# Kernel tuning notes

Measured on AMD Instinct MI355X. Metric: run time of the kernel, lower is better.

## Reference

```python
import jax, jax.numpy as jnp
import numpy as np

B_FACTOR = 4          # branching factor of the complete tree
DEPTH = 7             # levels 0..DEPTH; level DEPTH are leaves
N_NODES = (B_FACTOR ** (DEPTH + 1) - 1) // (B_FACTOR - 1)   # 21845
N_INTERNAL = (B_FACTOR ** DEPTH - 1) // (B_FACTOR - 1)      # 5461
IN_SIZE = 512
HID = 512
PARAM_SCALE = 0.02


def setup_inputs() -> dict:
    key = jax.random.key(0)
    ks = jax.random.split(key, 7)
    x = jax.random.normal(ks[0], (N_NODES, IN_SIZE), dtype=jnp.float32)
    # torch nn.Linear parameters: y = x @ W.T + b
    W_iou = jax.random.normal(ks[1], (3 * HID, IN_SIZE), dtype=jnp.float32) * PARAM_SCALE
    b_iou = jax.random.normal(ks[2], (3 * HID,), dtype=jnp.float32) * PARAM_SCALE
    W_f = jax.random.normal(ks[3], (HID, IN_SIZE), dtype=jnp.float32) * PARAM_SCALE
    b_f = jax.random.normal(ks[4], (HID,), dtype=jnp.float32) * PARAM_SCALE
    U_iou = jax.random.normal(ks[5], (3 * HID, HID), dtype=jnp.float32) * PARAM_SCALE
    U_f = jax.random.normal(ks[6], (HID, HID), dtype=jnp.float32) * PARAM_SCALE
    # children[j] = indices of the 4 children of internal node j (complete 4-ary tree)
    children = (B_FACTOR * jnp.arange(N_INTERNAL, dtype=jnp.int32)[:, None]
                + jnp.arange(1, B_FACTOR + 1, dtype=jnp.int32)[None, :])
    return {"x": x, "children": children, "W_iou": W_iou, "b_iou": b_iou,
            "W_f": W_f, "b_f": b_f, "U_iou": U_iou, "U_f": U_f}


def reference(x, children, W_iou, b_iou, W_f, b_f, U_iou, U_f):
    """Child-Sum Tree-LSTM over a complete 4-ary tree, processed level-batched
    bottom-up (equivalent to the per-node postorder recursion in the source).
    Leaves keep h = c = 0, as in the source (_forward_postorder returns early).
    NOTE: the source applies NO sigmoid to the forget gate term; we keep that.
    """
    N = x.shape[0]
    H = U_f.shape[0]
    # input-dependent parts are tree-independent: precompute once for all nodes
    wx_iou = x @ W_iou.T + b_iou          # [N, 3H]
    wx_f = x @ W_f.T + b_f                # [N, H]
    h = jnp.zeros((N, H), dtype=x.dtype)
    c = jnp.zeros_like(h)
    # level l occupies node indices [offs[l], offs[l+1]) — static constants
    offs = [(B_FACTOR ** l - 1) // (B_FACTOR - 1) for l in range(DEPTH + 2)]
    for l in range(DEPTH - 1, -1, -1):    # internal levels, deepest first
        s, e = offs[l], offs[l + 1]
        ch = children[s:e]                # [M, 4]
        h_ch = h[ch]                      # [M, 4, H] gather of child hidden states
        c_ch = c[ch]                      # [M, 4, H]
        h_sum = h_ch.sum(axis=1)          # child-sum
        iou = wx_iou[s:e] + h_sum @ U_iou.T               # [M, 3H]
        i, o, u = jnp.split(iou, 3, axis=-1)
        i = jax.nn.sigmoid(i)
        o = jax.nn.sigmoid(o)
        u = jnp.tanh(u)
        # forget term per child (no sigmoid, faithful to source)
        f = wx_f[s:e][:, None, :] + h_ch @ U_f.T          # [M, 4, H]
        c_new = i * u + (f * c_ch).sum(axis=1)            # [M, H]
        h = h.at[s:e].set(o * jnp.tanh(c_new))
        c = c.at[s:e].set(c_new)
    return h, c
```

## Files before the change

kernel.cpp:

```cpp
#include <hip/hip_runtime.h>
#include <cmath>

constexpr int N_NODES = 21845;
constexpr int N_INT   = 5461;
constexpr int HID     = 512;

typedef short  short8  __attribute__((ext_vector_type(8)));
typedef float  floatx4 __attribute__((ext_vector_type(4)));

__device__ __forceinline__ unsigned short f2bf(float f) {
    unsigned int u = __float_as_uint(f);
    u += 0x7fffu + ((u >> 16) & 1u);
    return (unsigned short)(u >> 16);
}

__global__ void prep_kernel(const float* __restrict__ x,
                            const float* __restrict__ W_iou,
                            const float* __restrict__ W_f,
                            const float* __restrict__ U_iou,
                            const float* __restrict__ U_f,
                            float* __restrict__ h_leaf,
                            float* __restrict__ c_leaf,
                            unsigned short* __restrict__ dstb)
{
    const size_t Z  = (size_t)(N_NODES - N_INT) * HID / 4;
    const size_t C0 = (size_t)N_INT * 512 / 4;
    const size_t C1 = C0 + 1536 * 512 / 4;
    const size_t C2 = C1 + 512 * 512 / 4;
    const size_t C3 = C2 + 1536 * 512 / 4;
    const size_t C4 = C3 + 512 * 512 / 4;
    const size_t total = 2 * Z + C4;
    size_t i = (size_t)blockIdx.x * blockDim.x + threadIdx.x;
    const size_t stride = (size_t)gridDim.x * blockDim.x;
    const float4 zz = {0.f, 0.f, 0.f, 0.f};
    for (; i < total; i += stride) {
        if (i < 2 * Z) {
            if (i < Z) ((float4*)h_leaf)[i] = zz;
            else       ((float4*)c_leaf)[i - Z] = zz;
        } else {
            size_t k = i - 2 * Z;
            const float* src; size_t off;
            if (k < C0)      { src = x;     off = k; }
            else if (k < C1) { src = W_iou; off = k - C0; }
            else if (k < C2) { src = W_f;   off = k - C1; }
            else if (k < C3) { src = U_iou; off = k - C2; }
            else             { src = U_f;   off = k - C3; }
            float4 v = ((const float4*)src)[off];
            ushort4 o;
            o.x = f2bf(v.x); o.y = f2bf(v.y); o.z = f2bf(v.z); o.w = f2bf(v.w);
            ((ushort4*)dstb)[k] = o;
        }
    }
}

#define GLD_LDS(g, l) __builtin_amdgcn_global_load_lds( \
    (const __attribute__((address_space(1))) void*)(g), \
    (__attribute__((address_space(3))) void*)(l), 16, 0, 0)

__device__ __forceinline__ void gemm_tile_128(
    const unsigned short* __restrict__ A, int Arows,
    const unsigned short* __restrict__ B,
    const float* __restrict__ bias,
    float* __restrict__ C, int ldc,
    int bm, int bn)
{
    __shared__ short8 AsV[1024];
    __shared__ short8 BsV[1024];

    const int tid  = threadIdx.x;
    const int wave = tid >> 6;
    const int lane = tid & 63;
    const int quad = lane >> 4;
    const int lr   = lane & 15;
    const int wr = (wave >> 1) * 64;
    const int wc = (wave & 1) * 64;

    floatx4 acc[4][4];
    #pragma unroll
    for (int i = 0; i < 4; ++i)
        #pragma unroll
        for (int j = 0; j < 4; ++j)
            acc[i][j] = (floatx4){0.f, 0.f, 0.f, 0.f};

    int s_row[4], s_gk[4];
    #pragma unroll
    for (int it = 0; it < 4; ++it) {
        int c = it * 256 + wave * 64 + lane;
        s_row[it] = c >> 3;
        s_gk[it]  = (c & 7) ^ (s_row[it] & 7);
    }

    for (int k0 = 0; k0 < 512; k0 += 64) {
        #pragma unroll
        for (int it = 0; it < 4; ++it) {
            int row = s_row[it];
            int gm = bm + row; if (gm >= Arows) gm = Arows - 1;
            GLD_LDS(A + (size_t)gm * 512 + k0 + s_gk[it] * 8, &AsV[it * 256 + wave * 64]);
            int gn = bn + row;
            GLD_LDS(B + (size_t)gn * 512 + k0 + s_gk[it] * 8, &BsV[it * 256 + wave * 64]);
        }
        __syncthreads();

        #pragma unroll
        for (int kc = 0; kc < 2; ++kc) {
            short8 af[4], bfr[4];
            const int q = kc * 4 + quad;
            #pragma unroll
            for (int mt = 0; mt < 4; ++mt) {
                int row = wr + mt * 16 + lr;
                af[mt] = AsV[row * 8 + (q ^ (row & 7))];
            }
            #pragma unroll
            for (int nt = 0; nt < 4; ++nt) {
                int row = wc + nt * 16 + lr;
                bfr[nt] = BsV[row * 8 + (q ^ (row & 7))];
            }
            #pragma unroll
            for (int mt = 0; mt < 4; ++mt)
                #pragma unroll
                for (int nt = 0; nt < 4; ++nt)
                    acc[mt][nt] = __builtin_amdgcn_mfma_f32_16x16x32_bf16(
                        af[mt], bfr[nt], acc[mt][nt], 0, 0, 0);
        }
        __syncthreads();
    }

    #pragma unroll
    for (int mt = 0; mt < 4; ++mt) {
        #pragma unroll
        for (int r = 0; r < 4; ++r) {
            int gm = bm + wr + mt * 16 + quad * 4 + r;
            if (gm >= Arows) continue;
            #pragma unroll
            for (int nt = 0; nt < 4; ++nt) {
                int gn = bn + wc + nt * 16 + lr;
                float v = acc[mt][nt][r];
                if (bias) v += bias[gn];
                C[(size_t)gm * ldc + gn] = v;
            }
        }
    }
}

__global__ __launch_bounds__(256) void wgemm_kernel(
    const unsigned short* __restrict__ xb,
    const unsigned short* __restrict__ Wib,
    const unsigned short* __restrict__ Wfb,
    const float* __restrict__ b_iou, const float* __restrict__ b_f,
    float* __restrict__ wx_iou, float* __restrict__ wx_f)
{
    int b = blockIdx.x;
    if (b < 516) {
        gemm_tile_128(xb, N_INT, Wib, b_iou, wx_iou, 1536, (b / 12) * 128, (b % 12) * 128);
    } else {
        int b2 = b - 516;
        gemm_tile_128(xb, 1365, Wfb, b_f, wx_f, 512, (b2 / 4) * 128, (b2 % 4) * 128);
    }
}

__global__ __launch_bounds__(256) void gemm5_kernel(
    const unsigned short* __restrict__ hs_bf,
    const unsigned short* __restrict__ h6_bf,
    const unsigned short* __restrict__ Uib, const unsigned short* __restrict__ Ufb,
    float* __restrict__ ioud, float* __restrict__ fd)
{
    int b = blockIdx.x;
    if (b < 96) {
        gemm_tile_128(hs_bf, 1024, Uib, nullptr, ioud, 1536, (b / 12) * 128, (b % 12) * 128);
    } else {
        int b2 = b - 96;
        gemm_tile_128(h6_bf, 4096, Ufb, nullptr, fd, 512, (b2 / 4) * 128, (b2 % 4) * 128);
    }
}

__global__ __launch_bounds__(256) void gemm4_kernel(
    const unsigned short* __restrict__ hs_bf,
    const unsigned short* __restrict__ h5_bf,
    const unsigned short* __restrict__ Uib, const unsigned short* __restrict__ Ufb,
    float* __restrict__ ioud, float* __restrict__ fd)
{
    int b = blockIdx.x;
    if (b < 24) {
        gemm_tile_128(hs_bf, 256, Uib, nullptr, ioud, 1536, (b / 12) * 128, (b % 12) * 128);
    } else {
        int b2 = b - 24;
        gemm_tile_128(h5_bf, 1024, Ufb, nullptr, fd, 512, (b2 / 4) * 128, (b2 % 4) * 128);
    }
}

__device__ __forceinline__ void direct_tile_16x64(
    const unsigned short* __restrict__ A, int Arows,
    const unsigned short* __restrict__ B,
    float* __restrict__ C, int ldc,
    int m0, int n0)
{
    const int lane = threadIdx.x & 63;
    const int quad = lane >> 4;
    const int lr   = lane & 15;
    int am = m0 + lr; if (am >= Arows) am = Arows - 1;
    const unsigned short* ap = A + (size_t)am * 512 + quad * 8;
    const unsigned short* bp = B + (size_t)(n0 + lr) * 512 + quad * 8;

    floatx4 acc[4];
    #pragma unroll
    for (int j = 0; j < 4; ++j) acc[j] = (floatx4){0.f, 0.f, 0.f, 0.f};

    #pragma unroll
    for (int k0 = 0; k0 < 512; k0 += 32) {
        short8 af = *(const short8*)(ap + k0);
        #pragma unroll
        for (int j = 0; j < 4; ++j) {
            short8 bf = *(const short8*)(bp + (size_t)j * 16 * 512 + k0);
            acc[j] = __builtin_amdgcn_mfma_f32_16x16x32_bf16(af, bf, acc[j], 0, 0, 0);
        }
    }

    #pragma unroll
    for (int j = 0; j < 4; ++j) {
        #pragma unroll
        for (int r = 0; r < 4; ++r) {
            int gm = m0 + quad * 4 + r;
            if (gm < Arows) C[(size_t)gm * ldc + n0 + j * 16 + lr] = acc[j][r];
        }
    }
}

__global__ __launch_bounds__(256) void gemm_small_kernel(
    const unsigned short* __restrict__ hs_bf,
    const unsigned short* __restrict__ hch_bf,
    const unsigned short* __restrict__ Uib, const unsigned short* __restrict__ Ufb,
    float* __restrict__ ioud, float* __restrict__ fd, int nl)
{
    const int w = blockIdx.x * 4 + (threadIdx.x >> 6);
    const int mI = (nl + 15) >> 4;
    const int nI = 1536 / 64;
    const int mF = (4 * nl + 15) >> 4;
    if (w < mI * nI) {
        direct_tile_16x64(hs_bf, nl, Uib, ioud, 1536, (w / nI) * 16, (w % nI) * 64);
    } else {
        int w2 = w - mI * nI;
        if (w2 < mF * 8)
            direct_tile_16x64(hch_bf, 4 * nl, Ufb, fd, 512, (w2 / 8) * 16, (w2 % 8) * 64);
    }
}

__global__ __launch_bounds__(512) void combine_wide_kernel(
    const float* __restrict__ wx_iou, const float* __restrict__ wx_f,
    const float* __restrict__ ioud, const float* __restrict__ fd,
    const float* __restrict__ c_child,
    float* __restrict__ h_out, float* __restrict__ c_out,
    unsigned short* __restrict__ h_bf, unsigned short* __restrict__ hs_bf,
    int s, int np)
{
    __shared__ float4 hsbuf[512];
    const int k  = threadIdx.x >> 7;
    const int jg = threadIdx.x & 127;
    const int j4 = jg << 2;
    const bool hasU = (ioud != nullptr);

    for (int tp = blockIdx.x; tp < np; tp += gridDim.x) {
        const int t = 4 * tp + k;
        const int n = s + t;
        const float* wrow = wx_iou + (size_t)n * 1536 + j4;
        float4 iv = *(const float4*)(wrow);
        float4 ov = *(const float4*)(wrow + 512);
        float4 uv = *(const float4*)(wrow + 1024);
        float4 fc = {0.f, 0.f, 0.f, 0.f};
        if (hasU) {
            const float* drow = ioud + (size_t)t * 1536 + j4;
            float4 a  = *(const float4*)(drow);
            float4 b  = *(const float4*)(drow + 512);
            float4 u2 = *(const float4*)(drow + 1024);
            float4 wf = *(const float4*)(wx_f + (size_t)n * 512 + j4);
            #pragma unroll
            for (int c = 0; c < 4; ++c) {
                ((float*)&iv)[c] += ((float*)&a)[c];
                ((float*)&ov)[c] += ((float*)&b)[c];
                ((float*)&uv)[c] += ((float*)&u2)[c];
            }
            #pragma unroll
            for (int q = 0; q < 4; ++q) {
                float4 f  = *(const float4*)(fd + (size_t)(4 * t + q) * 512 + j4);
                float4 cv = *(const float4*)(c_child + (size_t)(4 * t + q) * 512 + j4);
                #pragma unroll
                for (int c = 0; c < 4; ++c)
                    ((float*)&fc)[c] += (((float*)&wf)[c] + ((float*)&f)[c]) * ((float*)&cv)[c];
            }
        }
        float4 cn, hn; ushort4 hb;
        #pragma unroll
        for (int c = 0; c < 4; ++c) {
            float ig = 1.f / (1.f + expf(-((float*)&iv)[c]));
            float og = 1.f / (1.f + expf(-((float*)&ov)[c]));
            float ug = tanhf(((float*)&uv)[c]);
            float cv2 = ig * ug + ((float*)&fc)[c];
            float hv = og * tanhf(cv2);
            ((float*)&cn)[c] = cv2;
            ((float*)&hn)[c] = hv;
            ((unsigned short*)&hb)[c] = f2bf(hv);
        }
        *(float4*)(c_out + (size_t)n * 512 + j4) = cn;
        *(float4*)(h_out + (size_t)n * 512 + j4) = hn;
        *(ushort4*)(h_bf + (size_t)n * 512 + j4) = hb;
        hsbuf[threadIdx.x] = hn;
        __syncthreads();
        if (threadIdx.x < 128) {
            float4 s0 = hsbuf[jg], s1 = hsbuf[128 + jg], s2 = hsbuf[256 + jg], s3 = hsbuf[384 + jg];
            ushort4 ho;
            #pragma unroll
            for (int c = 0; c < 4; ++c)
                ((unsigned short*)&ho)[c] =
                    f2bf(((float*)&s0)[c] + ((float*)&s1)[c] + ((float*)&s2)[c] + ((float*)&s3)[c]);
            *(ushort4*)(hs_bf + (size_t)tp * 512 + j4) = ho;
        }
        __syncthreads();
    }
}

__global__ __launch_bounds__(128) void combine_root_kernel(
    const float* __restrict__ wx_iou, const float* __restrict__ wx_f,
    const float* __restrict__ ioud, const float* __restrict__ fd,
    const float* __restrict__ c_child,
    float* __restrict__ h_out, float* __restrict__ c_out)
{
    const int j4 = threadIdx.x << 2;
    float4 iv = *(const float4*)(wx_iou + j4);
    float4 ov = *(const float4*)(wx_iou + 512 + j4);
    float4 uv = *(const float4*)(wx_iou + 1024 + j4);
    float4 a  = *(const float4*)(ioud + j4);
    float4 b  = *(const float4*)(ioud + 512 + j4);
    float4 u2 = *(const float4*)(ioud + 1024 + j4);
    float4 wf = *(const float4*)(wx_f + j4);
    float4 fc = {0.f, 0.f, 0.f, 0.f};
    #pragma unroll
    for (int c = 0; c < 4; ++c) {
        ((float*)&iv)[c] += ((float*)&a)[c];
        ((float*)&ov)[c] += ((float*)&b)[c];
        ((float*)&uv)[c] += ((float*)&u2)[c];
    }
    #pragma unroll
    for (int q = 0; q < 4; ++q) {
        float4 f  = *(const float4*)(fd + (size_t)q * 512 + j4);
        float4 cv = *(const float4*)(c_child + (size_t)q * 512 + j4);
        #pragma unroll
        for (int c = 0; c < 4; ++c)
            ((float*)&fc)[c] += (((float*)&wf)[c] + ((float*)&f)[c]) * ((float*)&cv)[c];
    }
    float4 cn, hn;
    #pragma unroll
    for (int c = 0; c < 4; ++c) {
        float ig = 1.f / (1.f + expf(-((float*)&iv)[c]));
        float og = 1.f / (1.f + expf(-((float*)&ov)[c]));
        float ug = tanhf(((float*)&uv)[c]);
        float cv2 = ig * ug + ((float*)&fc)[c];
        ((float*)&cn)[c] = cv2;
        ((float*)&hn)[c] = og * tanhf(cv2);
    }
    *(float4*)(c_out + j4) = cn;
    *(float4*)(h_out + j4) = hn;
}

extern "C" void kernel_launch(void* const* d_in, const int* in_sizes, int n_in,
                              void* d_out, int out_size, void* d_ws, size_t ws_size,
                              hipStream_t stream) {
    const float* x     = (const float*)d_in[0];
    const float* W_iou = (const float*)d_in[2];
    const float* b_iou = (const float*)d_in[3];
    const float* W_f   = (const float*)d_in[4];
    const float* b_f   = (const float*)d_in[5];
    const float* U_iou = (const float*)d_in[6];
    const float* U_f   = (const float*)d_in[7];

    float* h_out = (float*)d_out;
    float* c_out = h_out + (size_t)N_NODES * HID;

    float* ws     = (float*)d_ws;
    float* wx_iou = ws;
    float* wx_f   = wx_iou + (size_t)N_INT * 1536;
    float* ioud   = wx_f   + (size_t)1365 * 512;
    float* fd     = ioud   + (size_t)1024 * 1536;
    unsigned short* xb   = (unsigned short*)(fd + (size_t)4096 * 512);
    unsigned short* Wib  = xb  + (size_t)N_INT * 512;
    unsigned short* Wfb  = Wib + (size_t)1536 * 512;
    unsigned short* Uib  = Wfb + (size_t)512 * 512;
    unsigned short* Ufb  = Uib + (size_t)1536 * 512;
    unsigned short* h_bf = Ufb + (size_t)512 * 512;
    unsigned short* hs_bf= h_bf + (size_t)N_INT * 512;

    const int offs[9] = {0, 1, 5, 21, 85, 341, 1365, 5461, 21845};

    prep_kernel<<<2048, 256, 0, stream>>>(x, W_iou, W_f, U_iou, U_f,
                                          h_out + (size_t)N_INT * HID,
                                          c_out + (size_t)N_INT * HID, xb);

    wgemm_kernel<<<516 + 44, 256, 0, stream>>>(xb, Wib, Wfb, b_iou, b_f, wx_iou, wx_f);

    combine_wide_kernel<<<1024, 512, 0, stream>>>(
        wx_iou, nullptr, nullptr, nullptr, nullptr,
        h_out, c_out, h_bf, hs_bf, 1365, 1024);

    gemm5_kernel<<<224, 256, 0, stream>>>(hs_bf, h_bf + (size_t)1365 * HID, Uib, Ufb, ioud, fd);
    combine_wide_kernel<<<256, 512, 0, stream>>>(
        wx_iou, wx_f, ioud, fd, c_out + (size_t)1365 * HID,
        h_out, c_out, h_bf, hs_bf, 341, 256);

    gemm4_kernel<<<56, 256, 0, stream>>>(hs_bf, h_bf + (size_t)341 * HID, Uib, Ufb, ioud, fd);
    combine_wide_kernel<<<64, 512, 0, stream>>>(
        wx_iou, wx_f, ioud, fd, c_out + (size_t)341 * HID,
        h_out, c_out, h_bf, hs_bf, 85, 64);

    for (int l = 3; l >= 1; --l) {
        const int s  = offs[l];
        const int nl = offs[l + 1] - s;
        const int cb = offs[l + 1];
        const int mI = (nl + 15) >> 4;
        const int mF = (4 * nl + 15) >> 4;
        const int waves = mI * 24 + mF * 8;
        gemm_small_kernel<<<(waves + 3) / 4, 256, 0, stream>>>(
            hs_bf, h_bf + (size_t)cb * HID, Uib, Ufb, ioud, fd, nl);
        combine_wide_kernel<<<(nl + 3) / 4, 512, 0, stream>>>(
            wx_iou, wx_f, ioud, fd, c_out + (size_t)cb * HID,
            h_out, c_out, h_bf, hs_bf, s, nl >> 2);
    }

    gemm_small_kernel<<<8, 256, 0, stream>>>(
        hs_bf, h_bf + (size_t)1 * HID, Uib, Ufb, ioud, fd, 1);
    combine_root_kernel<<<1, 128, 0, stream>>>(
        wx_iou, wx_f, ioud, fd, c_out + (size_t)1 * HID, h_out, c_out);
}
```

Measured before the change: 275.2 us.

## Fuse per-level GEMM and combine into single kernels, merge tail levels

Each internal level's U-GEMM and combine step now run in one kernel, with each block owning 16 parents' GEMM tiles and its own combine. The last three levels collapse into one single-block kernel, and the U weight conversion plus leaf zeroing move into the level-6 combine kernel. This removes many small launches and inter-kernel gaps on the serial bottom-up chain. In exchange, the large level-5 GEMM now runs as 64 blocks using the direct 16x64 MFMA path instead of 128x128 LDS-tiled tiles, which may lower throughput there. Ping-pong hs buffers are added so a level's child-sum input is not overwritten while it is being read.

```diff
diff --git a/kernel.cpp b/kernel.cpp
--- a/kernel.cpp
+++ b/kernel.cpp
@@ -14,42 +14,25 @@
     return (unsigned short)(u >> 16);
 }
 
-__global__ void prep_kernel(const float* __restrict__ x,
-                            const float* __restrict__ W_iou,
-                            const float* __restrict__ W_f,
-                            const float* __restrict__ U_iou,
-                            const float* __restrict__ U_f,
-                            float* __restrict__ h_leaf,
-                            float* __restrict__ c_leaf,
-                            unsigned short* __restrict__ dstb)
-{
-    const size_t Z  = (size_t)(N_NODES - N_INT) * HID / 4;
+__global__ void prep_a_kernel(const float* __restrict__ x,
+                              const float* __restrict__ W_iou,
+                              const float* __restrict__ W_f,
+                              unsigned short* __restrict__ dstb)
+{
     const size_t C0 = (size_t)N_INT * 512 / 4;
     const size_t C1 = C0 + 1536 * 512 / 4;
     const size_t C2 = C1 + 512 * 512 / 4;
-    const size_t C3 = C2 + 1536 * 512 / 4;
-    const size_t C4 = C3 + 512 * 512 / 4;
-    const size_t total = 2 * Z + C4;
     size_t i = (size_t)blockIdx.x * blockDim.x + threadIdx.x;
     const size_t stride = (size_t)gridDim.x * blockDim.x;
-    const float4 zz = {0.f, 0.f, 0.f, 0.f};
-    for (; i < total; i += stride) {
-        if (i < 2 * Z) {
-            if (i < Z) ((float4*)h_leaf)[i] = zz;
-            else       ((float4*)c_leaf)[i - Z] = zz;
-        } else {
-            size_t k = i - 2 * Z;
-            const float* src; size_t off;
-            if (k < C0)      { src = x;     off = k; }
-            else if (k < C1) { src = W_iou; off = k - C0; }
-            else if (k < C2) { src = W_f;   off = k - C1; }
-            else if (k < C3) { src = U_iou; off = k - C2; }
-            else             { src = U_f;   off = k - C3; }
-            float4 v = ((const float4*)src)[off];
-            ushort4 o;
-            o.x = f2bf(v.x); o.y = f2bf(v.y); o.z = f2bf(v.z); o.w = f2bf(v.w);
-            ((ushort4*)dstb)[k] = o;
-        }
+    for (; i < C2; i += stride) {
+        const float* src; size_t off;
+        if (i < C0)      { src = x;     off = i; }
+        else if (i < C1) { src = W_iou; off = i - C0; }
+        else             { src = W_f;   off = i - C1; }
+        float4 v = ((const float4*)src)[off];
+        ushort4 o;
+        o.x = f2bf(v.x); o.y = f2bf(v.y); o.z = f2bf(v.z); o.w = f2bf(v.w);
+        ((ushort4*)dstb)[i] = o;
     }
 }
 
@@ -158,33 +141,74 @@
     }
 }
 
-__global__ __launch_bounds__(256) void gemm5_kernel(
-    const unsigned short* __restrict__ hs_bf,
-    const unsigned short* __restrict__ h6_bf,
-    const unsigned short* __restrict__ Uib, const unsigned short* __restrict__ Ufb,
-    float* __restrict__ ioud, float* __restrict__ fd)
-{
-    int b = blockIdx.x;
-    if (b < 96) {
-        gemm_tile_128(hs_bf, 1024, Uib, nullptr, ioud, 1536, (b / 12) * 128, (b % 12) * 128);
-    } else {
-        int b2 = b - 96;
-        gemm_tile_128(h6_bf, 4096, Ufb, nullptr, fd, 512, (b2 / 4) * 128, (b2 % 4) * 128);
-    }
-}
-
-__global__ __launch_bounds__(256) void gemm4_kernel(
-    const unsigned short* __restrict__ hs_bf,
-    const unsigned short* __restrict__ h5_bf,
-    const unsigned short* __restrict__ Uib, const unsigned short* __restrict__ Ufb,
-    float* __restrict__ ioud, float* __restrict__ fd)
-{
-    int b = blockIdx.x;
-    if (b < 24) {
-        gemm_tile_128(hs_bf, 256, Uib, nullptr, ioud, 1536, (b / 12) * 128, (b % 12) * 128);
-    } else {
-        int b2 = b - 24;
-        gemm_tile_128(h5_bf, 1024, Ufb, nullptr, fd, 512, (b2 / 4) * 128, (b2 % 4) * 128);
+__global__ __launch_bounds__(512) void combine6_kernel(
+    const float* __restrict__ wx_iou,
+    const float* __restrict__ U_iou, const float* __restrict__ U_f,
+    float* __restrict__ h_out, float* __restrict__ c_out,
+    unsigned short* __restrict__ h_bf, unsigned short* __restrict__ hs_out,
+    unsigned short* __restrict__ Ub_dst,
+    float* __restrict__ h_leaf, float* __restrict__ c_leaf)
+{
+    __shared__ float4 hsbuf[512];
+    const int k  = threadIdx.x >> 7;
+    const int jg = threadIdx.x & 127;
+    const int j4 = jg << 2;
+
+    for (int tp = blockIdx.x; tp < 1024; tp += gridDim.x) {
+        const int n = 1365 + 4 * tp + k;
+        const float* wrow = wx_iou + (size_t)n * 1536 + j4;
+        float4 iv = *(const float4*)(wrow);
+        float4 ov = *(const float4*)(wrow + 512);
+        float4 uv = *(const float4*)(wrow + 1024);
+        float4 cn, hn; ushort4 hb;
+        #pragma unroll
+        for (int c = 0; c < 4; ++c) {
+            float ig = 1.f / (1.f + expf(-((float*)&iv)[c]));
+            float og = 1.f / (1.f + expf(-((float*)&ov)[c]));
+            float ug = tanhf(((float*)&uv)[c]);
+            float cv2 = ig * ug;
+            float hv = og * tanhf(cv2);
+            ((float*)&cn)[c] = cv2;
+            ((float*)&hn)[c] = hv;
+            ((unsigned short*)&hb)[c] = f2bf(hv);
+        }
+        *(float4*)(c_out + (size_t)n * 512 + j4) = cn;
+        *(float4*)(h_out + (size_t)n * 512 + j4) = hn;
+        *(ushort4*)(h_bf + (size_t)n * 512 + j4) = hb;
+        hsbuf[threadIdx.x] = hn;
+        __syncthreads();
+        if (threadIdx.x < 128) {
+            float4 s0 = hsbuf[jg], s1 = hsbuf[128 + jg], s2 = hsbuf[256 + jg], s3 = hsbuf[384 + jg];
+            ushort4 ho;
+            #pragma unroll
+            for (int c = 0; c < 4; ++c)
+                ((unsigned short*)&ho)[c] =
+                    f2bf(((float*)&s0)[c] + ((float*)&s1)[c] + ((float*)&s2)[c] + ((float*)&s3)[c]);
+            *(ushort4*)(hs_out + (size_t)tp * 512 + j4) = ho;
+        }
+        __syncthreads();
+    }
+
+    const size_t CU0 = (size_t)1536 * 512 / 4;
+    const size_t CU  = CU0 + (size_t)512 * 512 / 4;
+    const size_t Z   = (size_t)(N_NODES - N_INT) * HID / 4;
+    const size_t total = CU + 2 * Z;
+    const float4 zz = {0.f, 0.f, 0.f, 0.f};
+    for (size_t i = (size_t)blockIdx.x * blockDim.x + threadIdx.x; i < total;
+         i += (size_t)gridDim.x * blockDim.x) {
+        if (i < CU) {
+            const float* src; size_t off;
+            if (i < CU0) { src = U_iou; off = i; }
+            else         { src = U_f;   off = i - CU0; }
+            float4 v = ((const float4*)src)[off];
+            ushort4 o;
+            o.x = f2bf(v.x); o.y = f2bf(v.y); o.z = f2bf(v.z); o.w = f2bf(v.w);
+            ((ushort4*)Ub_dst)[i] = o;
+        } else {
+            size_t z = i - CU;
+            if (z < Z) ((float4*)h_leaf)[z] = zz;
+            else       ((float4*)c_leaf)[z - Z] = zz;
+        }
     }
 }
 
@@ -225,112 +249,23 @@
     }
 }
 
-__global__ __launch_bounds__(256) void gemm_small_kernel(
-    const unsigned short* __restrict__ hs_bf,
-    const unsigned short* __restrict__ hch_bf,
-    const unsigned short* __restrict__ Uib, const unsigned short* __restrict__ Ufb,
-    float* __restrict__ ioud, float* __restrict__ fd, int nl)
-{
-    const int w = blockIdx.x * 4 + (threadIdx.x >> 6);
-    const int mI = (nl + 15) >> 4;
-    const int nI = 1536 / 64;
-    const int mF = (4 * nl + 15) >> 4;
-    if (w < mI * nI) {
-        direct_tile_16x64(hs_bf, nl, Uib, ioud, 1536, (w / nI) * 16, (w % nI) * 64);
-    } else {
-        int w2 = w - mI * nI;
-        if (w2 < mF * 8)
-            direct_tile_16x64(hch_bf, 4 * nl, Ufb, fd, 512, (w2 / 8) * 16, (w2 % 8) * 64);
-    }
-}
-
-__global__ __launch_bounds__(512) void combine_wide_kernel(
+__device__ __forceinline__ void combine_item(
     const float* __restrict__ wx_iou, const float* __restrict__ wx_f,
     const float* __restrict__ ioud, const float* __restrict__ fd,
     const float* __restrict__ c_child,
     float* __restrict__ h_out, float* __restrict__ c_out,
-    unsigned short* __restrict__ h_bf, unsigned short* __restrict__ hs_bf,
-    int s, int np)
-{
-    __shared__ float4 hsbuf[512];
-    const int k  = threadIdx.x >> 7;
-    const int jg = threadIdx.x & 127;
-    const int j4 = jg << 2;
-    const bool hasU = (ioud != nullptr);
-
-    for (int tp = blockIdx.x; tp < np; tp += gridDim.x) {
-        const int t = 4 * tp + k;
-        const int n = s + t;
-        const float* wrow = wx_iou + (size_t)n * 1536 + j4;
-        float4 iv = *(const float4*)(wrow);
-        float4 ov = *(const float4*)(wrow + 512);
-        float4 uv = *(const float4*)(wrow + 1024);
-        float4 fc = {0.f, 0.f, 0.f, 0.f};
-        if (hasU) {
-            const float* drow = ioud + (size_t)t * 1536 + j4;
-            float4 a  = *(const float4*)(drow);
-            float4 b  = *(const float4*)(drow + 512);
-            float4 u2 = *(const float4*)(drow + 1024);
-            float4 wf = *(const float4*)(wx_f + (size_t)n * 512 + j4);
-            #pragma unroll
-            for (int c = 0; c < 4; ++c) {
-                ((float*)&iv)[c] += ((float*)&a)[c];
-                ((float*)&ov)[c] += ((float*)&b)[c];
-                ((float*)&uv)[c] += ((float*)&u2)[c];
-            }
-            #pragma unroll
-            for (int q = 0; q < 4; ++q) {
-                float4 f  = *(const float4*)(fd + (size_t)(4 * t + q) * 512 + j4);
-                float4 cv = *(const float4*)(c_child + (size_t)(4 * t + q) * 512 + j4);
-                #pragma unroll
-                for (int c = 0; c < 4; ++c)
-                    ((float*)&fc)[c] += (((float*)&wf)[c] + ((float*)&f)[c]) * ((float*)&cv)[c];
-            }
-        }
-        float4 cn, hn; ushort4 hb;
-        #pragma unroll
-        for (int c = 0; c < 4; ++c) {
-            float ig = 1.f / (1.f + expf(-((float*)&iv)[c]));
-            float og = 1.f / (1.f + expf(-((float*)&ov)[c]));
-            float ug = tanhf(((float*)&uv)[c]);
-            float cv2 = ig * ug + ((float*)&fc)[c];
-            float hv = og * tanhf(cv2);
-            ((float*)&cn)[c] = cv2;
-            ((float*)&hn)[c] = hv;
-            ((unsigned short*)&hb)[c] = f2bf(hv);
-        }
-        *(float4*)(c_out + (size_t)n * 512 + j4) = cn;
-        *(float4*)(h_out + (size_t)n * 512 + j4) = hn;
-        *(ushort4*)(h_bf + (size_t)n * 512 + j4) = hb;
-        hsbuf[threadIdx.x] = hn;
-        __syncthreads();
-        if (threadIdx.x < 128) {
-            float4 s0 = hsbuf[jg], s1 = hsbuf[128 + jg], s2 = hsbuf[256 + jg], s3 = hsbuf[384 + jg];
-            ushort4 ho;
-            #pragma unroll
-            for (int c = 0; c < 4; ++c)
-                ((unsigned short*)&ho)[c] =
-                    f2bf(((float*)&s0)[c] + ((float*)&s1)[c] + ((float*)&s2)[c] + ((float*)&s3)[c]);
-            *(ushort4*)(hs_bf + (size_t)tp * 512 + j4) = ho;
-        }
-        __syncthreads();
-    }
-}
-
-__global__ __launch_bounds__(128) void combine_root_kernel(
-    const float* __restrict__ wx_iou, const float* __restrict__ wx_f,
-    const float* __restrict__ ioud, const float* __restrict__ fd,
-    const float* __restrict__ c_child,
-    float* __restrict__ h_out, float* __restrict__ c_out)
-{
-    const int j4 = threadIdx.x << 2;
-    float4 iv = *(const float4*)(wx_iou + j4);
-    float4 ov = *(const float4*)(wx_iou + 512 + j4);
-    float4 uv = *(const float4*)(wx_iou + 1024 + j4);
-    float4 a  = *(const float4*)(ioud + j4);
-    float4 b  = *(const float4*)(ioud + 512 + j4);
-    float4 u2 = *(const float4*)(ioud + 1024 + j4);
-    float4 wf = *(const float4*)(wx_f + j4);
+    unsigned short* __restrict__ h_bf,
+    int n, int t, int j4, float4* hn_out)
+{
+    const float* wrow = wx_iou + (size_t)n * 1536 + j4;
+    float4 iv = *(const float4*)(wrow);
+    float4 ov = *(const float4*)(wrow + 512);
+    float4 uv = *(const float4*)(wrow + 1024);
+    const float* drow = ioud + (size_t)t * 1536 + j4;
+    float4 a  = *(const float4*)(drow);
+    float4 b  = *(const float4*)(drow + 512);
+    float4 u2 = *(const float4*)(drow + 1024);
+    float4 wf = *(const float4*)(wx_f + (size_t)n * 512 + j4);
     float4 fc = {0.f, 0.f, 0.f, 0.f};
     #pragma unroll
     for (int c = 0; c < 4; ++c) {
@@ -340,24 +275,145 @@
     }
     #pragma unroll
     for (int q = 0; q < 4; ++q) {
-        float4 f  = *(const float4*)(fd + (size_t)q * 512 + j4);
-        float4 cv = *(const float4*)(c_child + (size_t)q * 512 + j4);
+        float4 f  = *(const float4*)(fd + (size_t)(4 * t + q) * 512 + j4);
+        float4 cv = *(const float4*)(c_child + (size_t)(4 * t + q) * 512 + j4);
         #pragma unroll
         for (int c = 0; c < 4; ++c)
             ((float*)&fc)[c] += (((float*)&wf)[c] + ((float*)&f)[c]) * ((float*)&cv)[c];
     }
-    float4 cn, hn;
+    float4 cn, hn; ushort4 hb;
     #pragma unroll
     for (int c = 0; c < 4; ++c) {
         float ig = 1.f / (1.f + expf(-((float*)&iv)[c]));
         float og = 1.f / (1.f + expf(-((float*)&ov)[c]));
         float ug = tanhf(((float*)&uv)[c]);
         float cv2 = ig * ug + ((float*)&fc)[c];
+        float hv = og * tanhf(cv2);
         ((float*)&cn)[c] = cv2;
-        ((float*)&hn)[c] = og * tanhf(cv2);
-    }
-    *(float4*)(c_out + j4) = cn;
-    *(float4*)(h_out + j4) = hn;
+        ((float*)&hn)[c] = hv;
+        ((unsigned short*)&hb)[c] = f2bf(hv);
+    }
+    *(float4*)(c_out + (size_t)n * 512 + j4) = cn;
+    *(float4*)(h_out + (size_t)n * 512 + j4) = hn;
+    *(ushort4*)(h_bf + (size_t)n * 512 + j4) = hb;
+    *hn_out = hn;
+}
+
+__global__ __launch_bounds__(512) void fused_level_kernel(
+    const float* __restrict__ wx_iou, const float* __restrict__ wx_f,
+    const unsigned short* __restrict__ Uib, const unsigned short* __restrict__ Ufb,
+    const unsigned short* __restrict__ hs_in,
+    const unsigned short* __restrict__ hch_bf,
+    const float* __restrict__ c_child,
+    float* __restrict__ ioud, float* __restrict__ fd,
+    float* __restrict__ h_out, float* __restrict__ c_out,
+    unsigned short* __restrict__ h_bf, unsigned short* __restrict__ hs_out,
+    int s, int nl)
+{
+    const int b = blockIdx.x;
+    const int wave = threadIdx.x >> 6;
+
+    for (int tt = wave; tt < 56; tt += 8) {
+        if (tt < 24) {
+            direct_tile_16x64(hs_in, nl, Uib, ioud, 1536, 16 * b, tt * 64);
+        } else {
+            int ft = tt - 24;
+            direct_tile_16x64(hch_bf, 4 * nl, Ufb, fd, 512,
+                              64 * b + (ft >> 3) * 16, (ft & 7) * 64);
+        }
+    }
+    __syncthreads();
+
+    __shared__ float4 hsbuf[512];
+    const int k  = threadIdx.x >> 7;
+    const int jg = threadIdx.x & 127;
+    const int j4 = jg << 2;
+    for (int g = 0; g < 4; ++g) {
+        const int gp = 4 * b + g;
+        const int t  = 4 * gp + k;
+        float4 hn;
+        combine_item(wx_iou, wx_f, ioud, fd, c_child, h_out, c_out, h_bf,
+                     s + t, t, j4, &hn);
+        hsbuf[threadIdx.x] = hn;
+        __syncthreads();
+        if (threadIdx.x < 128) {
+            float4 s0 = hsbuf[jg], s1 = hsbuf[128 + jg], s2 = hsbuf[256 + jg], s3 = hsbuf[384 + jg];
+            ushort4 ho;
+            #pragma unroll
+            for (int c = 0; c < 4; ++c)
+                ((unsigned short*)&ho)[c] =
+                    f2bf(((float*)&s0)[c] + ((float*)&s1)[c] + ((float*)&s2)[c] + ((float*)&s3)[c]);
+            *(ushort4*)(hs_out + (size_t)gp * 512 + j4) = ho;
+        }
+        __syncthreads();
+    }
+}
+
+__global__ __launch_bounds__(1024) void tail3_kernel(
+    const float* __restrict__ wx_iou, const float* __restrict__ wx_f,
+    const unsigned short* __restrict__ Uib, const unsigned short* __restrict__ Ufb,
+    float* __restrict__ ioud, float* __restrict__ fd,
+    float* __restrict__ h_out, float* __restrict__ c_out,
+    unsigned short* __restrict__ h_bf,
+    unsigned short* __restrict__ hsA, unsigned short* __restrict__ hsB)
+{
+    __shared__ float4 hbuf[16 * 128];
+    const int wave = threadIdx.x >> 6;
+    const int tid  = threadIdx.x;
+
+    const int SS[3] = {5, 1, 0};
+    const int NL[3] = {16, 4, 1};
+    const int CB[3] = {21, 5, 1};
+    const unsigned short* hs_in[3] = {hsB, hsA, hsB};
+    unsigned short* hs_o[3] = {hsA, hsB, nullptr};
+
+    for (int li = 0; li < 3; ++li) {
+        const int s = SS[li], nl = NL[li], cb = CB[li];
+
+        const int mF = (4 * nl + 15) >> 4;
+        const int nT = 24 + mF * 8;
+        for (int tt = wave; tt < nT; tt += 16) {
+            if (tt < 24) {
+                direct_tile_16x64(hs_in[li], nl, Uib, ioud, 1536, 0, tt * 64);
+            } else {
+                int ft = tt - 24;
+                direct_tile_16x64(h_bf + (size_t)cb * 512, 4 * nl, Ufb, fd, 512,
+                                  (ft >> 3) * 16, (ft & 7) * 64);
+            }
+        }
+        __syncthreads();
+
+        const float* cch = c_out + (size_t)cb * 512;
+        for (int idx = tid; idx < nl * 128; idx += 1024) {
+            const int t  = idx >> 7;
+            const int jg = idx & 127;
+            const int j4 = jg << 2;
+            float4 hn;
+            combine_item(wx_iou, wx_f, ioud, fd, cch, h_out, c_out, h_bf,
+                         s + t, t, j4, &hn);
+            hbuf[idx] = hn;
+        }
+        __syncthreads();
+
+        if (hs_o[li]) {
+            for (int idx = tid; idx < (nl >> 2) * 128; idx += 1024) {
+                const int gp = idx >> 7;
+                const int jg = idx & 127;
+                const int j4 = jg << 2;
+                float4 s0 = hbuf[(4 * gp) * 128 + jg];
+                float4 s1 = hbuf[(4 * gp + 1) * 128 + jg];
+                float4 s2 = hbuf[(4 * gp + 2) * 128 + jg];
+                float4 s3 = hbuf[(4 * gp + 3) * 128 + jg];
+                ushort4 ho;
+                #pragma unroll
+                for (int c = 0; c < 4; ++c)
+                    ((unsigned short*)&ho)[c] =
+                        f2bf(((float*)&s0)[c] + ((float*)&s1)[c] + ((float*)&s2)[c] + ((float*)&s3)[c]);
+                *(ushort4*)(hs_o[li] + (size_t)gp * 512 + j4) = ho;
+            }
+        }
+        __syncthreads();
+    }
 }
 
 extern "C" void kernel_launch(void* const* d_in, const int* in_sizes, int n_in,
@@ -385,46 +441,27 @@
     unsigned short* Uib  = Wfb + (size_t)512 * 512;
     unsigned short* Ufb  = Uib + (size_t)1536 * 512;
     unsigned short* h_bf = Ufb + (size_t)512 * 512;
-    unsigned short* hs_bf= h_bf + (size_t)N_INT * 512;
-
-    const int offs[9] = {0, 1, 5, 21, 85, 341, 1365, 5461, 21845};
-
-    prep_kernel<<<2048, 256, 0, stream>>>(x, W_iou, W_f, U_iou, U_f,
-                                          h_out + (size_t)N_INT * HID,
-                                          c_out + (size_t)N_INT * HID, xb);
+    unsigned short* hsA  = h_bf + (size_t)N_INT * 512;
+    unsigned short* hsB  = hsA  + (size_t)1024 * 512;
+
+    prep_a_kernel<<<1024, 256, 0, stream>>>(x, W_iou, W_f, xb);
 
     wgemm_kernel<<<516 + 44, 256, 0, stream>>>(xb, Wib, Wfb, b_iou, b_f, wx_iou, wx_f);
 
-    combine_wide_kernel<<<1024, 512, 0, stream>>>(
-        wx_iou, nullptr, nullptr, nullptr, nullptr,
-        h_out, c_out, h_bf, hs_bf, 1365, 1024);
-
-    gemm5_kernel<<<224, 256, 0, stream>>>(hs_bf, h_bf + (size_t)1365 * HID, Uib, Ufb, ioud, fd);
-    combine_wide_kernel<<<256, 512, 0, stream>>>(
-        wx_iou, wx_f, ioud, fd, c_out + (size_t)1365 * HID,
-        h_out, c_out, h_bf, hs_bf, 341, 256);
-
-    gemm4_kernel<<<56, 256, 0, stream>>>(hs_bf, h_bf + (size_t)341 * HID, Uib, Ufb, ioud, fd);
-    combine_wide_kernel<<<64, 512, 0, stream>>>(
-        wx_iou, wx_f, ioud, fd, c_out + (size_t)341 * HID,
-        h_out, c_out, h_bf, hs_bf, 85, 64);
-
-    for (int l = 3; l >= 1; --l) {
-        const int s  = offs[l];
-        const int nl = offs[l + 1] - s;
-        const int cb = offs[l + 1];
-        const int mI = (nl + 15) >> 4;
-        const int mF = (4 * nl + 15) >> 4;
-        const int waves = mI * 24 + mF * 8;
-        gemm_small_kernel<<<(waves + 3) / 4, 256, 0, stream>>>(
-            hs_bf, h_bf + (size_t)cb * HID, Uib, Ufb, ioud, fd, nl);
-        combine_wide_kernel<<<(nl + 3) / 4, 512, 0, stream>>>(
-            wx_iou, wx_f, ioud, fd, c_out + (size_t)cb * HID,
-            h_out, c_out, h_bf, hs_bf, s, nl >> 2);
-    }
-
-    gemm_small_kernel<<<8, 256, 0, stream>>>(
-        hs_bf, h_bf + (size_t)1 * HID, Uib, Ufb, ioud, fd, 1);
-    combine_root_kernel<<<1, 128, 0, stream>>>(
-        wx_iou, wx_f, ioud, fd, c_out + (size_t)1 * HID, h_out, c_out);
-}
+    combine6_kernel<<<1024, 512, 0, stream>>>(
+        wx_iou, U_iou, U_f, h_out, c_out, h_bf, hsA, Uib,
+        h_out + (size_t)N_INT * HID, c_out + (size_t)N_INT * HID);
+
+    fused_level_kernel<<<64, 512, 0, stream>>>(
+        wx_iou, wx_f, Uib, Ufb, hsA, h_bf + (size_t)1365 * HID,
+        c_out + (size_t)1365 * HID, ioud, fd, h_out, c_out, h_bf, hsB, 341, 1024);
+    fused_level_kernel<<<16, 512, 0, stream>>>(
+        wx_iou, wx_f, Uib, Ufb, hsB, h_bf + (size_t)341 * HID,
+        c_out + (size_t)341 * HID, ioud, fd, h_out, c_out, h_bf, hsA, 85, 256);
+    fused_level_kernel<<<4, 512, 0, stream>>>(
+        wx_iou, wx_f, Uib, Ufb, hsA, h_bf + (size_t)85 * HID,
+        c_out + (size_t)85 * HID, ioud, fd, h_out, c_out, h_bf, hsB, 21, 64);
+
+    tail3_kernel<<<1, 1024, 0, stream>>>(
+        wx_iou, wx_f, Uib, Ufb, ioud, fd, h_out, c_out, h_bf, hsA, hsB);
+}
```

Measured after the change: 845.7 us. 207% more time.
